# Performance work log

Measured on AMD Instinct MI355X. Metric: run time of the kernel, lower is better.

Reference implementation:

```python
import jax, jax.numpy as jnp
import numpy as np

RADIUS = 0.2
K_SAMPLES = 32
SPATIAL_STRIDE = 2
TEMPORAL_K = 3
BN_EPS = 1e-5


def setup_inputs() -> dict:
    key = jax.random.key(0)
    ks = jax.random.split(key, 5)
    B, L, N, C = 4, 8, 2048, 32
    mid, out = 64, 128
    xyzs = jax.random.uniform(ks[0], (B, L, N, 3), dtype=jnp.float32)
    features = jax.random.normal(ks[1], (B, L, C, N), dtype=jnp.float32)
    conv_d_w = jax.random.normal(ks[2], (mid, 3), dtype=jnp.float32) * 0.3
    conv_f_w = jax.random.normal(ks[3], (mid, C), dtype=jnp.float32) * 0.1
    bn_gamma = jnp.ones((TEMPORAL_K * mid,), jnp.float32)
    bn_beta = jnp.zeros((TEMPORAL_K * mid,), jnp.float32)
    temporal_w = jax.random.normal(ks[4], (out, TEMPORAL_K * mid), dtype=jnp.float32) * 0.05
    return {"xyzs": xyzs, "features": features, "conv_d_w": conv_d_w,
            "conv_f_w": conv_f_w, "bn_gamma": bn_gamma, "bn_beta": bn_beta,
            "temporal_w": temporal_w}


def _fps(xyz, m):
    # furthest point sampling: xyz (N,3) -> (m,) int32 indices, first index is 0
    n = xyz.shape[0]
    def body(carry, _):
        dists, last = carry
        d = jnp.sum((xyz - xyz[last]) ** 2, axis=-1)
        dists = jnp.minimum(dists, d)
        nxt = jnp.argmax(dists).astype(jnp.int32)
        return (dists, nxt), last
    init = (jnp.full((n,), jnp.finfo(xyz.dtype).max, xyz.dtype), jnp.array(0, jnp.int32))
    _, idx = jax.lax.scan(body, init, None, length=m)
    return idx


def _ball_query(anchor, neighbor):
    # anchor (M,3), neighbor (N,3) -> (M,K) int32; first K points within RADIUS,
    # missing slots filled with first valid index (0 if none), matching pointnet2.
    n = neighbor.shape[0]
    d2 = jnp.sum((anchor[:, None, :] - neighbor[None, :, :]) ** 2, axis=-1)  # (M,N)
    cand = jnp.where(d2 < RADIUS * RADIUS, jnp.arange(n, dtype=jnp.int32)[None, :], n)
    cand = jnp.sort(cand, axis=1)[:, :K_SAMPLES]  # first K in index order
    first = cand[:, 0]
    safe_first = jnp.where(first == n, 0, first)
    return jnp.where(cand == n, safe_first[:, None], cand)


def _group(pts, idx):
    # pts (BL, N, D), idx (BL, M, K) -> (BL, M, K, D)
    return jnp.take_along_axis(pts[:, None, :, :], idx[..., None], axis=2)


def _forward(xyzs, features, conv_d_w, conv_f_w, bn_gamma, bn_beta, temporal_w):
    B, L, N, _ = xyzs.shape
    C = features.shape[2]
    M = N // SPATIAL_STRIDE
    KM = bn_gamma.shape[0]  # TEMPORAL_K * mid

    # temporal zero padding [1,1]
    xp = jnp.concatenate([jnp.zeros((B, 1, N, 3), xyzs.dtype), xyzs,
                          jnp.zeros((B, 1, N, 3), xyzs.dtype)], axis=1)  # (B,L+2,N,3)
    fp = jnp.concatenate([jnp.zeros((B, 1, C, N), features.dtype), features,
                          jnp.zeros((B, 1, C, N), features.dtype)], axis=1)

    # anchors from each center frame t=1..L
    center = xp[:, 1:L + 1].reshape(B * L, N, 3)
    anchor_idx = jax.vmap(lambda x: _fps(x, M))(center)            # (BL, M)
    anchor = jnp.take_along_axis(center, anchor_idx[..., None], axis=1)  # (BL, M, 3)

    offset_feats = []
    for o in range(TEMPORAL_K):  # neighbor frames t-1, t, t+1
        nb = xp[:, o:o + L].reshape(B * L, N, 3)
        nf = jnp.swapaxes(fp[:, o:o + L].reshape(B * L, C, N), 1, 2)  # (BL,N,C)
        idx = jax.vmap(_ball_query)(anchor, nb)                      # (BL,M,K)
        g_xyz = _group(nb, idx)                                      # (BL,M,K,3)
        g_f = _group(nf, idx)                                        # (BL,M,K,C)
        disp = g_xyz - anchor[:, :, None, :]
        d_out = jnp.einsum('oc,bmkc->bmko', conv_d_w, disp)          # (BL,M,K,mid)
        f_out = jnp.einsum('oc,bmkc->bmko', conv_f_w, g_f)
        # multiplication aggregation + sum pooling over neighbors
        offset_feats.append(jnp.sum(f_out * d_out, axis=2))          # (BL,M,mid)

    x = jnp.concatenate(offset_feats, axis=-1)                       # (BL,M,KM)
    x = jnp.transpose(x.reshape(B, L, M, KM), (0, 1, 3, 2))          # (B,L,KM,M)

    # BatchNorm1d applied per frame (torch loop calls BN once per t): stats over (B, M)
    mean = jnp.mean(x, axis=(0, 3), keepdims=True)
    var = jnp.var(x, axis=(0, 3), keepdims=True)
    x = (x - mean) * jax.lax.rsqrt(var + BN_EPS)
    x = x * bn_gamma[None, None, :, None] + bn_beta[None, None, :, None]
    x = jax.nn.relu(x)

    new_features = jnp.einsum('ok,blkm->blom', temporal_w, x)        # (B,L,out,M)
    new_xyzs = anchor.reshape(B, L, M, 3)
    return new_xyzs, new_features


def reference(xyzs, features, conv_d_w, conv_f_w, bn_gamma, bn_beta, temporal_w):
    return _forward(xyzs, features, conv_d_w, conv_f_w, bn_gamma, bn_beta, temporal_w)
```

## Files before the change

### kernel.cpp

```cpp
#include <hip/hip_runtime.h>

#define NB_B 4
#define NB_L 8
#define NB_N 2048
#define NB_C 32
#define NB_M 1024

#define ANCH_OFF  0
#define FT_OFF    98304
#define XRAW_OFF  2195456
#define STATS_OFF 8486912

__device__ __forceinline__ double u2d(unsigned long long u) {
  return __longlong_as_double((long long)u);
}
__device__ __forceinline__ unsigned long long d2u(double d) {
  return (unsigned long long)__double_as_longlong(d);
}
__device__ __forceinline__ double pack_dk(float d, unsigned inv) {
  return u2d(((unsigned long long)__float_as_uint(d) << 32) | inv);
}

#define DPP_XOR1 0xB1
#define DPP_XOR2 0x4E
#define DPP_HMIR 0x141
#define DPP_MIR  0x140

template <int CTRL>
__device__ __forceinline__ double dpp_max_f64(double v) {
  int lo = __double2loint(v), hi = __double2hiint(v);
  int plo = __builtin_amdgcn_update_dpp(0, lo, CTRL, 0xF, 0xF, false);
  int phi = __builtin_amdgcn_update_dpp(0, hi, CTRL, 0xF, 0xF, false);
  return fmax(v, __hiloint2double(phi, plo));
}

#define FPS_T 512

__global__ __launch_bounds__(FPS_T) void fps_transpose_kernel(
    const float* __restrict__ xyzs, const float* __restrict__ features,
    float* __restrict__ ft, float* __restrict__ anchors,
    float* __restrict__ d_out) {
  __shared__ __align__(16) unsigned char smem[32 * 1024 + 512];
  int t = threadIdx.x;
  if (blockIdx.x >= 32) {
    float(*tile)[65] = (float(*)[65])smem;
    int tb = blockIdx.x - 32;
    int frame = tb >> 5;
    int n0 = (tb & 31) * 64;
    const float* src = features + (size_t)frame * NB_C * NB_N;
    if (t < 256) {
#pragma unroll
      for (int i = 0; i < 8; ++i) {
        int q = t + i * 256;
        int c = q >> 6, n = q & 63;
        tile[c][n] = src[c * NB_N + n0 + n];
      }
    }
    __syncthreads();
    if (t < 256) {
      float* dst = ft + ((size_t)frame * NB_N + n0) * NB_C;
      int n = t >> 2, c0 = (t & 3) * 8;
      float v[8];
#pragma unroll
      for (int i = 0; i < 8; ++i) v[i] = tile[c0 + i][n];
      float4 w0 = {v[0], v[1], v[2], v[3]};
      float4 w1 = {v[4], v[5], v[6], v[7]};
      *(float4*)(dst + n * NB_C + c0) = w0;
      *(float4*)(dst + n * NB_C + c0 + 4) = w1;
    }
    return;
  }
  float4* pos4 = (float4*)smem;
  unsigned long long* slots = (unsigned long long*)(smem + 32768);
  int cloud = blockIdx.x;
  int w = t >> 6;
  int lane = t & 63;
  const float* xyz = xyzs + (size_t)cloud * NB_N * 3;
  for (int i = t; i < NB_N; i += FPS_T) {
    float x = xyz[i * 3 + 0];
    float y = xyz[i * 3 + 1];
    float z = xyz[i * 3 + 2];
    pos4[i] = make_float4(x, y, z, 0.f);
  }
  __syncthreads();
  float px[4], py[4], pz[4];
  double Kd[4];
  unsigned inv[4];
#pragma unroll
  for (int j = 0; j < 4; ++j) {
    int n = j * FPS_T + t;
    float4 p = pos4[n];
    px[j] = p.x; py[j] = p.y; pz[j] = p.z;
    inv[j] = 0x7FFFFFFFu - (unsigned)n;
    Kd[j] = pack_dk(3.402823466e38f, inv[j]);
  }
  int last = 0;
  int h0 = 0, h1 = 0;
  float4 sp = pos4[0];
  float lx = sp.x, ly = sp.y, lz = sp.z;
  int sidx = w * 4 + (lane >> 4);
  bool swrite = (lane & 15) == 0;
  int t512 = t + 512;
  for (int m = 0; m < NB_M; ++m) {
    h0 = (m == t) ? last : h0;
    h1 = (m == t512) ? last : h1;
    int par = m & 1;
    double best = u2d(0ull);
#pragma unroll
    for (int j = 0; j < 4; ++j) {
      float dx = __fsub_rn(px[j], lx);
      float dy = __fsub_rn(py[j], ly);
      float dz = __fsub_rn(pz[j], lz);
      float d = __fadd_rn(__fadd_rn(__fmul_rn(dx, dx), __fmul_rn(dy, dy)),
                          __fmul_rn(dz, dz));
      Kd[j] = fmin(Kd[j], pack_dk(d, inv[j]));
      best = fmax(best, Kd[j]);
    }
    best = dpp_max_f64<DPP_XOR1>(best);
    best = dpp_max_f64<DPP_XOR2>(best);
    best = dpp_max_f64<DPP_HMIR>(best);
    best = dpp_max_f64<DPP_MIR>(best);
    if (swrite) slots[par * 32 + sidx] = d2u(best);
    __syncthreads();
    ulonglong2 pr2 = *(const ulonglong2*)&slots[par * 32 + (lane & 15) * 2];
    double g = fmax(u2d(pr2.x), u2d(pr2.y));
    g = dpp_max_f64<DPP_XOR1>(g);
    g = dpp_max_f64<DPP_XOR2>(g);
    g = dpp_max_f64<DPP_HMIR>(g);
    g = dpp_max_f64<DPP_MIR>(g);
    last = 0x7FFFFFFF - __double2loint(g);
    float4 p = pos4[last];
    lx = p.x; ly = p.y; lz = p.z;
  }
  {
    float4 p = pos4[h0];
    size_t o = ((size_t)cloud * NB_M + t) * 3;
    anchors[o + 0] = p.x; anchors[o + 1] = p.y; anchors[o + 2] = p.z;
    d_out[o + 0] = p.x;   d_out[o + 1] = p.y;   d_out[o + 2] = p.z;
    float4 q = pos4[h1];
    size_t o2 = ((size_t)cloud * NB_M + t512) * 3;
    anchors[o2 + 0] = q.x; anchors[o2 + 1] = q.y; anchors[o2 + 2] = q.z;
    d_out[o2 + 0] = q.x;   d_out[o2 + 1] = q.y;   d_out[o2 + 2] = q.z;
  }
}

__device__ __forceinline__ float rdlane(float v, int l) {
  return __int_as_float(__builtin_amdgcn_readlane(__float_as_int(v), l));
}

#define BQ_WAVES 4
#define BQ_TPW 4

__global__ __launch_bounds__(256) void bq_conv_kernel(
    const float* __restrict__ xyzs, const float* __restrict__ ft,
    const float* __restrict__ anchors, const float* __restrict__ conv_d_w,
    const float* __restrict__ conv_f_w, float* __restrict__ x_raw) {
  int w = threadIdx.x >> 6, lane = threadIdx.x & 63;
  int tid = threadIdx.x;
  int gw = blockIdx.x * BQ_WAVES + w;
  int task0 = gw * BQ_TPW;
  int cloud = task0 / 3072;
  int rem = task0 - cloud * 3072;
  int o = rem >> 10, m0 = rem & 1023;
  int b = cloud >> 3, l = cloud & 7;
  int nl = l + o - 1;
  __shared__ int list_s[BQ_WAVES][32];
  __shared__ __align__(16) float4 pos_l[NB_N];
  float* xbase = x_raw + ((size_t)(l * NB_B + b) * NB_M + m0) * 192 + o * 64;
  if (nl < 0 || nl >= NB_L) {
#pragma unroll
    for (int t4 = 0; t4 < BQ_TPW; ++t4) xbase[(size_t)t4 * 192 + lane] = 0.0f;
    return;
  }
  const float* nb = xyzs + (size_t)(b * NB_L + nl) * NB_N * 3;
  for (int i = tid; i < NB_N; i += 256) {
    float x = nb[i * 3 + 0], y = nb[i * 3 + 1], z = nb[i * 3 + 2];
    pos_l[i] = make_float4(x, y, z, 0.f);
  }
  __syncthreads();

  const float4* wf4 = (const float4*)(conv_f_w + lane * 32);
  float wf[32];
#pragma unroll
  for (int i = 0; i < 8; ++i) {
    float4 v = wf4[i];
    wf[i * 4 + 0] = v.x; wf[i * 4 + 1] = v.y;
    wf[i * 4 + 2] = v.z; wf[i * 4 + 3] = v.w;
  }
  float wd0 = conv_d_w[lane * 3 + 0];
  float wd1 = conv_d_w[lane * 3 + 1];
  float wd2 = conv_d_w[lane * 3 + 2];

  const float* ftf = ft + (size_t)(b * NB_L + nl) * NB_N * NB_C + (lane & 31);
  unsigned long long lmlt = (1ull << lane) - 1ull;
  int kbase = (lane >> 5) << 4;

  for (int t4 = 0; t4 < BQ_TPW; ++t4) {
    int m = m0 + t4;
    const float* ap = anchors + ((size_t)cloud * NB_M + m) * 3;
    float ax = ap[0], ay = ap[1], az = ap[2];

    int count = 0;
    for (int batch = 0; batch < 4; ++batch) {
      unsigned long long bm[8];
#pragma unroll
      for (int c2 = 0; c2 < 8; ++c2) {
        int n = batch * 512 + c2 * 64 + lane;
        float4 p = pos_l[n];
        float dx = __fsub_rn(ax, p.x);
        float dy = __fsub_rn(ay, p.y);
        float dz = __fsub_rn(az, p.z);
        float d2 = __fadd_rn(__fadd_rn(__fmul_rn(dx, dx), __fmul_rn(dy, dy)),
                             __fmul_rn(dz, dz));
        bm[c2] = __ballot(d2 < 0.04f);
      }
#pragma unroll
      for (int c2 = 0; c2 < 8; ++c2) {
        bool hit = (bm[c2] >> lane) & 1;
        int pos = count + __popcll(bm[c2] & lmlt);
        if (hit && pos < 32) list_s[w][pos] = batch * 512 + c2 * 64 + lane;
        count += __popcll(bm[c2]);
      }
      if (count >= 32) break;
    }
    asm volatile("s_waitcnt lgkmcnt(0)" ::: "memory");
    int cnt = count < 32 ? count : 32;
    int first = (cnt > 0) ? list_s[w][0] : 0;

    int k = lane & 31;
    int idxk = (k < cnt) ? list_s[w][k] : first;
    float4 pb = pos_l[idxk];
    float d0 = __fsub_rn(pb.x, ax);
    float d1 = __fsub_rn(pb.y, ay);
    float d2v = __fsub_rn(pb.z, az);

    float G0 = 0.f, G1 = 0.f, G2 = 0.f;
#pragma unroll 8
    for (int i = 0; i < 16; ++i) {
      int kk = kbase + i;
      int ik = (kk < cnt) ? list_s[w][kk] : first;
      float fv = ftf[(size_t)ik * NB_C];
      float e0 = __shfl(d0, kk);
      float e1 = __shfl(d1, kk);
      float e2 = __shfl(d2v, kk);
      G0 = fmaf(fv, e0, G0);
      G1 = fmaf(fv, e1, G1);
      G2 = fmaf(fv, e2, G2);
    }
    G0 += __shfl_xor(G0, 32);
    G1 += __shfl_xor(G1, 32);
    G2 += __shfl_xor(G2, 32);

    float acc = 0.f;
#pragma unroll
    for (int cc = 0; cc < 32; ++cc) {
      float g0 = rdlane(G0, cc);
      float g1 = rdlane(G1, cc);
      float g2 = rdlane(G2, cc);
      float tt = fmaf(g2, wd2, fmaf(g1, wd1, g0 * wd0));
      acc = fmaf(wf[cc], tt, acc);
    }
    xbase[(size_t)t4 * 192 + lane] = acc;
  }
}

__global__ __launch_bounds__(192) void bn_stats_kernel(const float* __restrict__ x_raw,
                                                       float* __restrict__ stats) {
  int bid = blockIdx.x;
  int mt = bid & 3, bb = (bid >> 2) & 3, l = bid >> 4;
  int c = threadIdx.x;
  const float* p = x_raw + ((size_t)(l * NB_B + bb) * NB_M + mt * 256) * 192 + c;
  float s = 0.f, s2 = 0.f;
  for (int i = 0; i < 256; ++i) {
    float v = p[(size_t)i * 192];
    s += v;
    s2 = fmaf(v, v, s2);
  }
  atomicAdd(&stats[l * 192 + c], s);
  atomicAdd(&stats[1536 + l * 192 + c], s2);
}

__global__ __launch_bounds__(256) void final_kernel(
    const float* __restrict__ x_raw, const float* __restrict__ stats,
    const float* __restrict__ gamma, const float* __restrict__ beta,
    const float* __restrict__ tw, float* __restrict__ out) {
  __shared__ __align__(16) float xn[32 * 192];
  __shared__ __align__(16) float wt[64 * 132];
  __shared__ float sc[192], sh[192];
  int cloud = blockIdx.x >> 5;
  int mt = blockIdx.x & 31;
  int b = cloud >> 3, l = cloud & 7;
  int m0 = mt * 32;
  int t = threadIdx.x;
  if (t < 192) {
    float mean = stats[l * 192 + t] * (1.0f / 4096.0f);
    float ex2 = stats[1536 + l * 192 + t] * (1.0f / 4096.0f);
    float var = fmaxf(ex2 - mean * mean, 0.0f);
    float g = gamma[t] / sqrtf(var + 1e-5f);
    sc[t] = g;
    sh[t] = fmaf(-mean, g, beta[t]);
  }
  __syncthreads();
  const float* xp = x_raw + ((size_t)(l * NB_B + b) * NB_M + m0) * 192;
#pragma unroll
  for (int i = 0; i < 24; ++i) {
    int q = t + i * 256;
    int cc = q % 192;
    float v = xp[q];
    xn[q] = fmaxf(fmaf(v, sc[cc], sh[cc]), 0.0f);
  }
  float acc[4][4];
#pragma unroll
  for (int i = 0; i < 4; ++i)
#pragma unroll
    for (int j = 0; j < 4; ++j) acc[i][j] = 0.f;
  int o0 = (t & 31) * 4;
  int mg = (t >> 5) * 4;
  for (int kt = 0; kt < 3; ++kt) {
    __syncthreads();
#pragma unroll
    for (int i = 0; i < 32; ++i) {
      int q = t + i * 256;
      int oo = q >> 6, kk = q & 63;
      wt[kk * 132 + oo] = tw[oo * 192 + kt * 64 + kk];
    }
    __syncthreads();
#pragma unroll
    for (int kk = 0; kk < 64; kk += 4) {
      float a[4][4], bb2[4][4];
#pragma unroll
      for (int mi = 0; mi < 4; ++mi) {
        float4 v = *(const float4*)&xn[(mg + mi) * 192 + kt * 64 + kk];
        a[mi][0] = v.x; a[mi][1] = v.y; a[mi][2] = v.z; a[mi][3] = v.w;
      }
#pragma unroll
      for (int j = 0; j < 4; ++j) {
        float4 v = *(const float4*)&wt[(kk + j) * 132 + o0];
        bb2[j][0] = v.x; bb2[j][1] = v.y; bb2[j][2] = v.z; bb2[j][3] = v.w;
      }
#pragma unroll
      for (int mi = 0; mi < 4; ++mi)
#pragma unroll
        for (int j = 0; j < 4; ++j)
#pragma unroll
          for (int oi = 0; oi < 4; ++oi)
            acc[mi][oi] = fmaf(a[mi][j], bb2[j][oi], acc[mi][oi]);
    }
  }
  float* op = out + 98304 + ((size_t)cloud * 128 + o0) * NB_M + m0 + mg;
#pragma unroll
  for (int oi = 0; oi < 4; ++oi) {
    float4 v = {acc[0][oi], acc[1][oi], acc[2][oi], acc[3][oi]};
    *(float4*)(op + (size_t)oi * NB_M) = v;
  }
}

extern "C" void kernel_launch(void* const* d_in, const int* in_sizes, int n_in,
                              void* d_out, int out_size, void* d_ws, size_t ws_size,
                              hipStream_t stream) {
  const float* xyzs = (const float*)d_in[0];
  const float* features = (const float*)d_in[1];
  const float* conv_d_w = (const float*)d_in[2];
  const float* conv_f_w = (const float*)d_in[3];
  const float* bn_gamma = (const float*)d_in[4];
  const float* bn_beta = (const float*)d_in[5];
  const float* temporal_w = (const float*)d_in[6];
  float* ws = (float*)d_ws;
  float* anchors = ws + ANCH_OFF;
  float* ft = ws + FT_OFF;
  float* xraw = ws + XRAW_OFF;
  float* stats = ws + STATS_OFF;
  float* out = (float*)d_out;

  hipMemsetAsync(stats, 0, 3072 * sizeof(float), stream);
  fps_transpose_kernel<<<1056, FPS_T, 0, stream>>>(xyzs, features, ft,
                                                   anchors, out);
  bq_conv_kernel<<<6144, 256, 0, stream>>>(xyzs, ft, anchors, conv_d_w,
                                           conv_f_w, xraw);
  bn_stats_kernel<<<128, 192, 0, stream>>>(xraw, stats);
  final_kernel<<<1024, 256, 0, stream>>>(xraw, stats, bn_gamma, bn_beta,
                                         temporal_w, out);
}
```

Before: 741.1 us.

## Pack two FPS clouds per block with 256 threads each

Each furthest-point-sampling block now processes two point clouds, each handled by four waves of 256 threads holding eight points per thread, and the FPS grid shrinks from 32 to 16 blocks. Selected indices are recorded in a shared-memory history and written out cooperatively at the end, replacing the per-thread register capture. The aim is to halve the number of FPS blocks and shorten the cross-wave reduction to four waves per cloud. In exchange, each thread does twice the distance work per iteration, and the two clouds share one block-wide barrier per step.

```diff
diff --git a/kernel.cpp b/kernel.cpp
--- a/kernel.cpp
+++ b/kernel.cpp
@@ -35,16 +35,20 @@
 }
 
 #define FPS_T 512
+#define FPS_BLOCKS 16
+
+#define SM_SLOTS 65536
+#define SM_HIST  66048
 
 __global__ __launch_bounds__(FPS_T) void fps_transpose_kernel(
     const float* __restrict__ xyzs, const float* __restrict__ features,
     float* __restrict__ ft, float* __restrict__ anchors,
     float* __restrict__ d_out) {
-  __shared__ __align__(16) unsigned char smem[32 * 1024 + 512];
+  __shared__ __align__(16) unsigned char smem[74240];
   int t = threadIdx.x;
-  if (blockIdx.x >= 32) {
+  if (blockIdx.x >= FPS_BLOCKS) {
     float(*tile)[65] = (float(*)[65])smem;
-    int tb = blockIdx.x - 32;
+    int tb = blockIdx.x - FPS_BLOCKS;
     int frame = tb >> 5;
     int n0 = (tb & 31) * 64;
     const float* src = features + (size_t)frame * NB_C * NB_N;
@@ -70,44 +74,45 @@
     }
     return;
   }
-  float4* pos4 = (float4*)smem;
-  unsigned long long* slots = (unsigned long long*)(smem + 32768);
-  int cloud = blockIdx.x;
   int w = t >> 6;
   int lane = t & 63;
+  int half = w >> 2;
+  int t256 = t & 255;
+  int w4 = w & 3;
+  int cloud = blockIdx.x * 2 + half;
+  float4* pos = ((float4*)smem) + half * NB_N;
+  unsigned long long* slots = (unsigned long long*)(smem + SM_SLOTS);
+  int* hist = (int*)(smem + SM_HIST) + half * NB_M;
   const float* xyz = xyzs + (size_t)cloud * NB_N * 3;
-  for (int i = t; i < NB_N; i += FPS_T) {
+  for (int i = t256; i < NB_N; i += 256) {
     float x = xyz[i * 3 + 0];
     float y = xyz[i * 3 + 1];
     float z = xyz[i * 3 + 2];
-    pos4[i] = make_float4(x, y, z, 0.f);
+    pos[i] = make_float4(x, y, z, 0.f);
   }
   __syncthreads();
-  float px[4], py[4], pz[4];
-  double Kd[4];
-  unsigned inv[4];
-#pragma unroll
-  for (int j = 0; j < 4; ++j) {
-    int n = j * FPS_T + t;
-    float4 p = pos4[n];
+  float px[8], py[8], pz[8];
+  double Kd[8];
+  unsigned inv[8];
+#pragma unroll
+  for (int j = 0; j < 8; ++j) {
+    int n = j * 256 + t256;
+    float4 p = pos[n];
     px[j] = p.x; py[j] = p.y; pz[j] = p.z;
     inv[j] = 0x7FFFFFFFu - (unsigned)n;
     Kd[j] = pack_dk(3.402823466e38f, inv[j]);
   }
   int last = 0;
-  int h0 = 0, h1 = 0;
-  float4 sp = pos4[0];
+  float4 sp = pos[0];
   float lx = sp.x, ly = sp.y, lz = sp.z;
-  int sidx = w * 4 + (lane >> 4);
+  int sidx = half * 16 + w4 * 4 + (lane >> 4);
   bool swrite = (lane & 15) == 0;
-  int t512 = t + 512;
   for (int m = 0; m < NB_M; ++m) {
-    h0 = (m == t) ? last : h0;
-    h1 = (m == t512) ? last : h1;
+    if (t256 == 0) hist[m] = last;
     int par = m & 1;
     double best = u2d(0ull);
 #pragma unroll
-    for (int j = 0; j < 4; ++j) {
+    for (int j = 0; j < 8; ++j) {
       float dx = __fsub_rn(px[j], lx);
       float dy = __fsub_rn(py[j], ly);
       float dz = __fsub_rn(pz[j], lz);
@@ -122,25 +127,23 @@
     best = dpp_max_f64<DPP_MIR>(best);
     if (swrite) slots[par * 32 + sidx] = d2u(best);
     __syncthreads();
-    ulonglong2 pr2 = *(const ulonglong2*)&slots[par * 32 + (lane & 15) * 2];
+    ulonglong2 pr2 =
+        *(const ulonglong2*)&slots[par * 32 + half * 16 + (lane & 7) * 2];
     double g = fmax(u2d(pr2.x), u2d(pr2.y));
     g = dpp_max_f64<DPP_XOR1>(g);
     g = dpp_max_f64<DPP_XOR2>(g);
     g = dpp_max_f64<DPP_HMIR>(g);
-    g = dpp_max_f64<DPP_MIR>(g);
     last = 0x7FFFFFFF - __double2loint(g);
-    float4 p = pos4[last];
+    float4 p = pos[last];
     lx = p.x; ly = p.y; lz = p.z;
   }
-  {
-    float4 p = pos4[h0];
-    size_t o = ((size_t)cloud * NB_M + t) * 3;
+  __syncthreads();
+  for (int mm = t256; mm < NB_M; mm += 256) {
+    int idx = hist[mm];
+    float4 p = pos[idx];
+    size_t o = ((size_t)cloud * NB_M + mm) * 3;
     anchors[o + 0] = p.x; anchors[o + 1] = p.y; anchors[o + 2] = p.z;
     d_out[o + 0] = p.x;   d_out[o + 1] = p.y;   d_out[o + 2] = p.z;
-    float4 q = pos4[h1];
-    size_t o2 = ((size_t)cloud * NB_M + t512) * 3;
-    anchors[o2 + 0] = q.x; anchors[o2 + 1] = q.y; anchors[o2 + 2] = q.z;
-    d_out[o2 + 0] = q.x;   d_out[o2 + 1] = q.y;   d_out[o2 + 2] = q.z;
   }
 }
 
@@ -373,7 +376,7 @@
   float* out = (float*)d_out;
 
   hipMemsetAsync(stats, 0, 3072 * sizeof(float), stream);
-  fps_transpose_kernel<<<1056, FPS_T, 0, stream>>>(xyzs, features, ft,
+  fps_transpose_kernel<<<1040, FPS_T, 0, stream>>>(xyzs, features, ft,
                                                    anchors, out);
   bq_conv_kernel<<<6144, 256, 0, stream>>>(xyzs, ft, anchors, conv_d_w,
                                            conv_f_w, xraw);
```

Result: slower. 844.9 us (+14.0%).
